# Kernel tuning notes

Hardware: AMD Instinct MI355X
Metric: run time of the kernel (lower is better)

## Reference

```python
import jax, jax.numpy as jnp
import numpy as np

B, N, C = 16384, 4, 512
H = 8
HD = C // H
WIN = 2
SCALE = HD ** -0.5
HID = 2048


def _rel_pos_index(w):
    # same construction as the torch buffer, done in numpy (constant)
    coords = np.stack(np.meshgrid(np.arange(w), np.arange(w), indexing='ij'))  # [2,w,w]
    flat = coords.reshape(2, -1)                      # [2, w*w]
    rel = flat[:, :, None] - flat[:, None, :]         # [2, N, N]
    rel = rel.transpose(1, 2, 0).astype(np.int64)     # [N, N, 2]
    rel[:, :, 0] += w - 1
    rel[:, :, 1] += w - 1
    rel[:, :, 0] *= 2 * w - 1
    return rel.sum(-1)                                # [N, N]

REL_IDX = _rel_pos_index(WIN)


def setup_inputs() -> dict:
    key = jax.random.key(0)
    ks = jax.random.split(key, 8)
    s = lambda fan: 1.0 / np.sqrt(fan)
    return {
        'x': jax.random.normal(ks[0], (B, N, C), jnp.float32),
        'ln_g': jnp.ones((C,), jnp.float32),
        'ln_b': jnp.zeros((C,), jnp.float32),
        'qkv_w': jax.random.normal(ks[1], (3 * C, C), jnp.float32) * s(C),
        'proj_w': jax.random.normal(ks[2], (C, C), jnp.float32) * s(C),
        'proj_b': jnp.zeros((C,), jnp.float32),
        'rpb_table': jax.random.normal(ks[3], ((2 * WIN - 1) ** 2, H), jnp.float32) * 0.02,
        'fc1_w': jax.random.normal(ks[4], (HID, C), jnp.float32) * s(C),
        'fc1_b': jnp.zeros((HID,), jnp.float32),
        'fc2_w': jax.random.normal(ks[5], (C, HID), jnp.float32) * s(HID),
        'fc2_b': jnp.zeros((C,), jnp.float32),
    }


def _layernorm(x, g, b, eps=1e-5):
    mu = jnp.mean(x, axis=-1, keepdims=True)
    var = jnp.mean(jnp.square(x - mu), axis=-1, keepdims=True)
    return (x - mu) * jax.lax.rsqrt(var + eps) * g + b


def reference(x, ln_g, ln_b, qkv_w, proj_w, proj_b, rpb_table, fc1_w, fc1_b, fc2_w, fc2_b):
    # --- attention branch (pre-norm, shared LayerNorm params) ---
    h = _layernorm(x, ln_g, ln_b)
    qkv = h @ qkv_w.T                                  # [B,N,3C]
    qkv = qkv.reshape(B, N, 3, H, HD).transpose(2, 0, 3, 1, 4)  # [3,B,H,N,HD]
    q, k, v = qkv[0], qkv[1], qkv[2]
    attn = jnp.einsum('bhnd,bhmd->bhnm', q, k) * SCALE  # [B,H,N,N]
    bias = rpb_table[REL_IDX.reshape(-1)].reshape(N, N, H).transpose(2, 0, 1)  # [H,N,N]
    attn = jax.nn.softmax(attn + bias[None], axis=-1)
    o = jnp.einsum('bhnm,bhmd->bhnd', attn, v)          # [B,H,N,HD]
    o = o.transpose(0, 2, 1, 3).reshape(B, N, C)
    o = o @ proj_w.T + proj_b
    x = x + o
    # --- MLP branch (same LayerNorm params reused, as in the torch code) ---
    h = _layernorm(x, ln_g, ln_b)
    h = jax.nn.gelu(h @ fc1_w.T + fc1_b, approximate=False)
    h = h @ fc2_w.T + fc2_b
    return x + h
```

## Files before the change

### kernel.cpp

```cpp
#include <hip/hip_runtime.h>
#include <hip/hip_bf16.h>
#include <math.h>

#define BQ   16384
#define CH   512
#define NH   8
#define HID  2048
#define NTOK (BQ*4)

using bf16 = __hip_bfloat16;
typedef __bf16 bf16x8 __attribute__((ext_vector_type(8)));
typedef float  f32x4  __attribute__((ext_vector_type(4)));

__device__ __forceinline__ void gload16(const void* g, void* l) {
    __builtin_amdgcn_global_load_lds(
        (const __attribute__((address_space(1))) void*)g,
        (__attribute__((address_space(3))) void*)l, 16, 0, 0);
}

__global__ __launch_bounds__(256) void packw(const float* __restrict__ Wsrc,
                                             bf16* __restrict__ out, int N, int K) {
    int q = blockIdx.x * 256 + threadIdx.x;
    int NSk = K >> 5;
    int total = (N >> 7) * NSk * 512;
    if (q >= total) return;
    int l  = q & 63;
    int jj = (q >> 6) & 1;
    int w  = (q >> 7) & 3;
    int s  = (q >> 9) % NSk;
    int cb = q / (NSk * 512);
    int row = cb * 128 + w * 32 + jj * 16 + (l >> 2);
    int k   = s * 32 + ((l & 3) ^ ((l >> 3) & 3)) * 8;
    const float* src = Wsrc + (size_t)row * K + k;
    float4 v0 = *(const float4*)src;
    float4 v1 = *(const float4*)(src + 4);
    __align__(16) bf16 t[8];
    t[0] = __float2bfloat16(v0.x); t[1] = __float2bfloat16(v0.y);
    t[2] = __float2bfloat16(v0.z); t[3] = __float2bfloat16(v0.w);
    t[4] = __float2bfloat16(v1.x); t[5] = __float2bfloat16(v1.y);
    t[6] = __float2bfloat16(v1.z); t[7] = __float2bfloat16(v1.w);
    *(uint4*)&out[(size_t)q * 8] = *(const uint4*)t;
}

__global__ __launch_bounds__(256) void ln_kernel(const float* __restrict__ x,
                                                 const float* __restrict__ g,
                                                 const float* __restrict__ b,
                                                 bf16* __restrict__ out) {
    int row  = blockIdx.x * 4 + (threadIdx.x >> 6);
    int lane = threadIdx.x & 63;
    const float* xr = x + (size_t)row * CH;
    int c0 = lane * 8;
    float4 v0 = *(const float4*)&xr[c0];
    float4 v1 = *(const float4*)&xr[c0 + 4];
    float s  = v0.x + v0.y + v0.z + v0.w + v1.x + v1.y + v1.z + v1.w;
    float sq = v0.x*v0.x + v0.y*v0.y + v0.z*v0.z + v0.w*v0.w
             + v1.x*v1.x + v1.y*v1.y + v1.z*v1.z + v1.w*v1.w;
#pragma unroll
    for (int off = 32; off >= 1; off >>= 1) {
        s  += __shfl_xor(s,  off, 64);
        sq += __shfl_xor(sq, off, 64);
    }
    float mu  = s * (1.0f / CH);
    float var = sq * (1.0f / CH) - mu * mu;
    float rs  = rsqrtf(var + 1e-5f);
    float4 g0 = *(const float4*)&g[c0];
    float4 g1 = *(const float4*)&g[c0 + 4];
    float4 b0 = *(const float4*)&b[c0];
    float4 b1 = *(const float4*)&b[c0 + 4];
    __align__(16) bf16 t[8];
    t[0] = __float2bfloat16((v0.x - mu) * rs * g0.x + b0.x);
    t[1] = __float2bfloat16((v0.y - mu) * rs * g0.y + b0.y);
    t[2] = __float2bfloat16((v0.z - mu) * rs * g0.z + b0.z);
    t[3] = __float2bfloat16((v0.w - mu) * rs * g0.w + b0.w);
    t[4] = __float2bfloat16((v1.x - mu) * rs * g1.x + b1.x);
    t[5] = __float2bfloat16((v1.y - mu) * rs * g1.y + b1.y);
    t[6] = __float2bfloat16((v1.z - mu) * rs * g1.z + b1.z);
    t[7] = __float2bfloat16((v1.w - mu) * rs * g1.w + b1.w);
    *(uint4*)&out[(size_t)row * CH + c0] = *(const uint4*)t;
}

template<int EPI>
__global__ __launch_bounds__(256, 3)
void gemm128(const bf16* __restrict__ A, const bf16* __restrict__ Bp,
             int M, int N, int K, int nbx,
             const float* __restrict__ bias,
             const float* resid, float* outF, bf16* __restrict__ outB) {
    __shared__ __align__(16) char lds[32768];
    const int tid  = threadIdx.x;
    const int w    = tid >> 6;
    const int lane = tid & 63;

    const int nb  = gridDim.x;
    const int id  = blockIdx.x;
    const int swz = (id & 7) * (nb >> 3) + (id >> 3);
    const int bx  = swz % nbx, by = swz / nbx;
    const int bm = by * 128, bn = bx * 128;
    const int wrh = w >> 1;
    const int wch = w & 1;
    const int NSk = K >> 5;

    const int rl  = lane >> 2;
    const int kpe = ((lane & 3) ^ ((lane >> 3) & 3)) * 8;
    const bf16* gA0 = A + (size_t)(bm + w * 32 + rl) * K + kpe;
    const bf16* gA1 = gA0 + (size_t)16 * K;
    const bf16* gB = Bp + (size_t)(bn >> 7) * NSk * 4096 + w * 1024 + lane * 8;

    const int kslot = ((lane >> 4) ^ ((lane >> 1) & 3));
    const int aoff = (wrh * 64 + (lane & 15)) * 64 + kslot * 16;
    const int boff = 8192 + (wch * 64 + (lane & 15)) * 64 + kslot * 16;

    f32x4 acc[4][4] = {};

    auto stage = [&](int s) {
        char* base = (char*)lds + (s & 1) * 16384;
        gload16(gA0 + (size_t)s * 32,         base + w * 2048);
        gload16(gA1 + (size_t)s * 32,         base + w * 2048 + 1024);
        gload16(gB  + (size_t)s * 4096,       base + 8192 + w * 2048);
        gload16(gB  + (size_t)s * 4096 + 512, base + 8192 + w * 2048 + 1024);
    };

    auto compute = [&](int slot) {
        const char* base = (const char*)lds + slot * 16384;
        bf16x8 av[4], bv[4];
#pragma unroll
        for (int n = 0; n < 4; ++n)
            bv[n] = *(const bf16x8*)(base + boff + n * 1024);
#pragma unroll
        for (int m = 0; m < 4; ++m)
            av[m] = *(const bf16x8*)(base + aoff + m * 1024);
#pragma unroll
        for (int m = 0; m < 4; ++m)
#pragma unroll
            for (int n = 0; n < 4; ++n)
                acc[m][n] = __builtin_amdgcn_mfma_f32_16x16x32_bf16(av[m], bv[n], acc[m][n], 0, 0, 0);
    };

    stage(0);
    __syncthreads();
    for (int s = 0; s < NSk - 1; ++s) {
        stage(s + 1);
        compute(s & 1);
        __syncthreads();
    }
    compute((NSk - 1) & 1);

    const int erow0 = bm + wrh * 64 + (lane >> 4) * 4;
    const int ecol0 = bn + wch * 64 + (lane & 15);
#pragma unroll
    for (int m = 0; m < 4; ++m) {
#pragma unroll
        for (int n = 0; n < 4; ++n) {
            int col = ecol0 + n * 16;
#pragma unroll
            for (int r = 0; r < 4; ++r) {
                int row = erow0 + m * 16 + r;
                size_t idx = (size_t)row * N + col;
                float v = acc[m][n][r];
                if (EPI == 0) {
                    outB[idx] = __float2bfloat16(v);
                } else if (EPI == 1) {
                    outF[idx] = v + bias[col] + resid[idx];
                } else {
                    float t = v + bias[col];
                    float u = 0.7978845608f * t * (1.0f + 0.044715f * t * t);
                    float e = __expf(2.0f * u);
                    float th = 1.0f - 2.0f / (e + 1.0f);
                    outB[idx] = __float2bfloat16(0.5f * t * (1.0f + th));
                }
            }
        }
    }
}

__global__ __launch_bounds__(256)
void attn_kernel(const bf16* __restrict__ qkv, const float* __restrict__ rpb,
                 bf16* __restrict__ o) {
    __shared__ __align__(16) bf16 sT[4 * 1536];
    __shared__ float sS[NH][4][4];
    __shared__ float sP[NH][4][4];
    int b   = blockIdx.x;
    int tid = threadIdx.x;
    const bf16* src = qkv + (size_t)b * (4 * 1536);
#pragma unroll
    for (int it = 0; it < 3; ++it) {
        int e = (it * 256 + tid) * 8;
        *(uint4*)&sT[e] = *(const uint4*)&src[e];
    }
    __syncthreads();
    if (tid < 128) {
        int h = tid >> 4, i = (tid >> 2) & 3, j = tid & 3;
        const bf16* q = &sT[i * 1536 + h * 64];
        const bf16* k = &sT[j * 1536 + 512 + h * 64];
        float acc = 0.f;
#pragma unroll
        for (int d = 0; d < 64; ++d)
            acc += __bfloat162float(q[d]) * __bfloat162float(k[d]);
        int rel = (((i >> 1) - (j >> 1)) + 1) * 3 + (((i & 1) - (j & 1)) + 1);
        sS[h][i][j] = acc * 0.125f + rpb[rel * NH + h];
    }
    __syncthreads();
    if (tid < 32) {
        int h = tid >> 2, i = tid & 3;
        float s0 = sS[h][i][0], s1 = sS[h][i][1], s2 = sS[h][i][2], s3 = sS[h][i][3];
        float mx = fmaxf(fmaxf(s0, s1), fmaxf(s2, s3));
        float e0 = expf(s0 - mx), e1 = expf(s1 - mx), e2 = expf(s2 - mx), e3 = expf(s3 - mx);
        float inv = 1.f / (e0 + e1 + e2 + e3);
        sP[h][i][0] = e0 * inv; sP[h][i][1] = e1 * inv;
        sP[h][i][2] = e2 * inv; sP[h][i][3] = e3 * inv;
    }
    __syncthreads();
    {
        int h = tid >> 5, tl = tid & 31;
        int d = tl * 2;
        const bf16* v = &sT[1024 + h * 64 + d];
#pragma unroll
        for (int i = 0; i < 4; ++i) {
            float p0 = sP[h][i][0], p1 = sP[h][i][1], p2 = sP[h][i][2], p3 = sP[h][i][3];
            float o0 = p0 * __bfloat162float(v[0])        + p1 * __bfloat162float(v[1536])
                     + p2 * __bfloat162float(v[2 * 1536]) + p3 * __bfloat162float(v[3 * 1536]);
            float o1 = p0 * __bfloat162float(v[1])            + p1 * __bfloat162float(v[1536 + 1])
                     + p2 * __bfloat162float(v[2 * 1536 + 1]) + p3 * __bfloat162float(v[3 * 1536 + 1]);
            __hip_bfloat162 pr;
            pr.x = __float2bfloat16(o0);
            pr.y = __float2bfloat16(o1);
            *(__hip_bfloat162*)&o[(size_t)(b * 4 + i) * CH + h * 64 + d] = pr;
        }
    }
}

extern "C" void kernel_launch(void* const* d_in, const int* in_sizes, int n_in,
                              void* d_out, int out_size, void* d_ws, size_t ws_size,
                              hipStream_t stream) {
    const float* x      = (const float*)d_in[0];
    const float* ln_g   = (const float*)d_in[1];
    const float* ln_b   = (const float*)d_in[2];
    const float* qkv_w  = (const float*)d_in[3];
    const float* proj_w = (const float*)d_in[4];
    const float* proj_b = (const float*)d_in[5];
    const float* rpb    = (const float*)d_in[6];
    const float* fc1_w  = (const float*)d_in[7];
    const float* fc1_b  = (const float*)d_in[8];
    const float* fc2_w  = (const float*)d_in[9];
    const float* fc2_b  = (const float*)d_in[10];
    float* out = (float*)d_out;

    char* ws = (char*)d_ws;
    bf16* wQKV  = (bf16*)ws;  ws += (size_t)1536 * 512 * 2;
    bf16* wPROJ = (bf16*)ws;  ws += (size_t)512  * 512 * 2;
    bf16* wFC1  = (bf16*)ws;  ws += (size_t)2048 * 512 * 2;
    bf16* wFC2  = (bf16*)ws;  ws += (size_t)512 * 2048 * 2;
    bf16* hA    = (bf16*)ws;  ws += (size_t)NTOK * 512 * 2;
    bf16* big   = (bf16*)ws;
    const size_t needed = 6291456ull + 67108864ull + 268435456ull;
    if (ws_size < needed) return;

    packw<<<384, 256, 0, stream>>>(qkv_w,  wQKV, 1536, 512);
    packw<<<128, 256, 0, stream>>>(proj_w, wPROJ, 512, 512);
    packw<<<512, 256, 0, stream>>>(fc1_w,  wFC1, 2048, 512);
    packw<<<512, 256, 0, stream>>>(fc2_w,  wFC2, 512, 2048);

    ln_kernel<<<NTOK / 4, 256, 0, stream>>>(x, ln_g, ln_b, hA);
    gemm128<0><<<dim3(12 * 512), 256, 0, stream>>>(
        hA, wQKV, NTOK, 1536, 512, 12, nullptr, nullptr, nullptr, big);
    attn_kernel<<<BQ, 256, 0, stream>>>(big, rpb, hA);
    gemm128<1><<<dim3(4 * 512), 256, 0, stream>>>(
        hA, wPROJ, NTOK, 512, 512, 4, proj_b, x, out, nullptr);
    ln_kernel<<<NTOK / 4, 256, 0, stream>>>(out, ln_g, ln_b, hA);
    gemm128<2><<<dim3(16 * 512), 256, 0, stream>>>(
        hA, wFC1, NTOK, 2048, 512, 16, fc1_b, nullptr, nullptr, big);
    gemm128<1><<<dim3(4 * 512), 256, 0, stream>>>(
        big, wFC2, NTOK, 512, 2048, 4, fc2_b, out, out, nullptr);
}
```

Measured before the change: 816.7 us.

## Load weight tiles directly to registers and use K=64 stages in GEMM

```diff
diff --git a/kernel.cpp b/kernel.cpp
--- a/kernel.cpp
+++ b/kernel.cpp
@@ -12,25 +12,26 @@
 typedef __bf16 bf16x8 __attribute__((ext_vector_type(8)));
 typedef float  f32x4  __attribute__((ext_vector_type(4)));
 
+#define FENCE() asm volatile("" ::: "memory")
+
 __device__ __forceinline__ void gload16(const void* g, void* l) {
     __builtin_amdgcn_global_load_lds(
         (const __attribute__((address_space(1))) void*)g,
         (__attribute__((address_space(3))) void*)l, 16, 0, 0);
 }
 
-__global__ __launch_bounds__(256) void packw(const float* __restrict__ Wsrc,
+__global__ __launch_bounds__(256) void packb(const float* __restrict__ Wsrc,
                                              bf16* __restrict__ out, int N, int K) {
     int q = blockIdx.x * 256 + threadIdx.x;
-    int NSk = K >> 5;
-    int total = (N >> 7) * NSk * 512;
+    int NSk32 = K >> 5;
+    int total = (N >> 7) * NSk32 * 512;
     if (q >= total) return;
-    int l  = q & 63;
-    int jj = (q >> 6) & 1;
-    int w  = (q >> 7) & 3;
-    int s  = (q >> 9) % NSk;
-    int cb = q / (NSk * 512);
-    int row = cb * 128 + w * 32 + jj * 16 + (l >> 2);
-    int k   = s * 32 + ((l & 3) ^ ((l >> 3) & 3)) * 8;
+    int l   = q & 63;
+    int nt  = (q >> 6) & 7;
+    int s32 = (q >> 9) % NSk32;
+    int cb  = q / (NSk32 * 512);
+    int row = cb * 128 + nt * 16 + (l & 15);
+    int k   = s32 * 32 + (l >> 4) * 8;
     const float* src = Wsrc + (size_t)row * K + k;
     float4 v0 = *(const float4*)src;
     float4 v1 = *(const float4*)(src + 4);
@@ -80,8 +81,8 @@
 }
 
 template<int EPI>
-__global__ __launch_bounds__(256, 3)
-void gemm128(const bf16* __restrict__ A, const bf16* __restrict__ Bp,
+__global__ __launch_bounds__(256, 4)
+void gemmk64(const bf16* __restrict__ A, const bf16* __restrict__ Bp,
              int M, int N, int K, int nbx,
              const float* __restrict__ bias,
              const float* resid, float* outF, bf16* __restrict__ outB) {
@@ -97,52 +98,73 @@
     const int bm = by * 128, bn = bx * 128;
     const int wrh = w >> 1;
     const int wch = w & 1;
-    const int NSk = K >> 5;
+    const int NS    = K >> 6;
+    const int NSk32 = K >> 5;
 
     const int rl  = lane >> 2;
     const int kpe = ((lane & 3) ^ ((lane >> 3) & 3)) * 8;
     const bf16* gA0 = A + (size_t)(bm + w * 32 + rl) * K + kpe;
     const bf16* gA1 = gA0 + (size_t)16 * K;
-    const bf16* gB = Bp + (size_t)(bn >> 7) * NSk * 4096 + w * 1024 + lane * 8;
+    const bf16* gB = Bp + (size_t)(bn >> 7) * NSk32 * 4096 + (wch * 4) * 512 + lane * 8;
 
     const int kslot = ((lane >> 4) ^ ((lane >> 1) & 3));
     const int aoff = (wrh * 64 + (lane & 15)) * 64 + kslot * 16;
-    const int boff = 8192 + (wch * 64 + (lane & 15)) * 64 + kslot * 16;
 
     f32x4 acc[4][4] = {};
-
-    auto stage = [&](int s) {
+    bf16x8 bvA[8], bvB[8];
+
+    auto stageA = [&](int s) {
         char* base = (char*)lds + (s & 1) * 16384;
-        gload16(gA0 + (size_t)s * 32,         base + w * 2048);
-        gload16(gA1 + (size_t)s * 32,         base + w * 2048 + 1024);
-        gload16(gB  + (size_t)s * 4096,       base + 8192 + w * 2048);
-        gload16(gB  + (size_t)s * 4096 + 512, base + 8192 + w * 2048 + 1024);
+        gload16(gA0 + (size_t)s * 64,      base + w * 2048);
+        gload16(gA1 + (size_t)s * 64,      base + w * 2048 + 1024);
+        gload16(gA0 + (size_t)s * 64 + 32, base + 8192 + w * 2048);
+        gload16(gA1 + (size_t)s * 64 + 32, base + 8192 + w * 2048 + 1024);
     };
 
-    auto compute = [&](int slot) {
-        const char* base = (const char*)lds + slot * 16384;
-        bf16x8 av[4], bv[4];
-#pragma unroll
-        for (int n = 0; n < 4; ++n)
-            bv[n] = *(const bf16x8*)(base + boff + n * 1024);
-#pragma unroll
-        for (int m = 0; m < 4; ++m)
-            av[m] = *(const bf16x8*)(base + aoff + m * 1024);
-#pragma unroll
-        for (int m = 0; m < 4; ++m)
-#pragma unroll
-            for (int n = 0; n < 4; ++n)
-                acc[m][n] = __builtin_amdgcn_mfma_f32_16x16x32_bf16(av[m], bv[n], acc[m][n], 0, 0, 0);
-    };
-
-    stage(0);
-    __syncthreads();
-    for (int s = 0; s < NSk - 1; ++s) {
-        stage(s + 1);
-        compute(s & 1);
-        __syncthreads();
-    }
-    compute((NSk - 1) & 1);
+#define LOADB(BV, S) {                                                       \
+    const bf16* _p = gB + (size_t)(2 * (S)) * 4096;                          \
+    BV[0] = *(const bf16x8*)(_p);        BV[1] = *(const bf16x8*)(_p + 512); \
+    BV[2] = *(const bf16x8*)(_p + 1024); BV[3] = *(const bf16x8*)(_p + 1536);\
+    BV[4] = *(const bf16x8*)(_p + 4096);        BV[5] = *(const bf16x8*)(_p + 4096 + 512); \
+    BV[6] = *(const bf16x8*)(_p + 4096 + 1024); BV[7] = *(const bf16x8*)(_p + 4096 + 1536); }
+
+#define COMPUTE(SLOT, BV) {                                                  \
+    const char* _b = (const char*)lds + (size_t)(SLOT) * 16384;              \
+    bf16x8 _av0[4], _av1[4];                                                 \
+    _Pragma("unroll") for (int _m = 0; _m < 4; ++_m) {                       \
+        _av0[_m] = *(const bf16x8*)(_b + aoff + _m * 1024);                  \
+        _av1[_m] = *(const bf16x8*)(_b + 8192 + aoff + _m * 1024); }         \
+    _Pragma("unroll") for (int _m = 0; _m < 4; ++_m)                         \
+    _Pragma("unroll") for (int _n = 0; _n < 4; ++_n)                         \
+        acc[_m][_n] = __builtin_amdgcn_mfma_f32_16x16x32_bf16(_av0[_m], BV[_n], acc[_m][_n], 0, 0, 0); \
+    _Pragma("unroll") for (int _m = 0; _m < 4; ++_m)                         \
+    _Pragma("unroll") for (int _n = 0; _n < 4; ++_n)                         \
+        acc[_m][_n] = __builtin_amdgcn_mfma_f32_16x16x32_bf16(_av1[_m], BV[4 + _n], acc[_m][_n], 0, 0, 0); }
+
+#define WAITV(n) asm volatile("s_waitcnt vmcnt(" #n ")" ::: "memory")
+#define SBAR()   __builtin_amdgcn_s_barrier()
+
+    stageA(0); LOADB(bvA, 0);
+    for (int s = 0; s < NS - 2; s += 2) {
+        stageA(s + 1); LOADB(bvB, s + 1);
+        WAITV(12); SBAR(); FENCE();
+        COMPUTE(s & 1, bvA);
+        FENCE(); SBAR();
+        stageA(s + 2); LOADB(bvA, s + 2);
+        WAITV(12); SBAR(); FENCE();
+        COMPUTE((s + 1) & 1, bvB);
+        FENCE(); SBAR();
+    }
+    stageA(NS - 1); LOADB(bvB, NS - 1);
+    WAITV(12); SBAR(); FENCE();
+    COMPUTE((NS - 2) & 1, bvA);
+    FENCE(); SBAR();
+    WAITV(0); SBAR(); FENCE();
+    COMPUTE((NS - 1) & 1, bvB);
+#undef LOADB
+#undef COMPUTE
+#undef WAITV
+#undef SBAR
 
     const int erow0 = bm + wrh * 64 + (lane >> 4) * 4;
     const int ecol0 = bn + wch * 64 + (lane & 15);
@@ -254,20 +276,20 @@
     const size_t needed = 6291456ull + 67108864ull + 268435456ull;
     if (ws_size < needed) return;
 
-    packw<<<384, 256, 0, stream>>>(qkv_w,  wQKV, 1536, 512);
-    packw<<<128, 256, 0, stream>>>(proj_w, wPROJ, 512, 512);
-    packw<<<512, 256, 0, stream>>>(fc1_w,  wFC1, 2048, 512);
-    packw<<<512, 256, 0, stream>>>(fc2_w,  wFC2, 512, 2048);
+    packb<<<384, 256, 0, stream>>>(qkv_w,  wQKV, 1536, 512);
+    packb<<<128, 256, 0, stream>>>(proj_w, wPROJ, 512, 512);
+    packb<<<512, 256, 0, stream>>>(fc1_w,  wFC1, 2048, 512);
+    packb<<<512, 256, 0, stream>>>(fc2_w,  wFC2, 512, 2048);
 
     ln_kernel<<<NTOK / 4, 256, 0, stream>>>(x, ln_g, ln_b, hA);
-    gemm128<0><<<dim3(12 * 512), 256, 0, stream>>>(
+    gemmk64<0><<<dim3(12 * 512), 256, 0, stream>>>(
         hA, wQKV, NTOK, 1536, 512, 12, nullptr, nullptr, nullptr, big);
     attn_kernel<<<BQ, 256, 0, stream>>>(big, rpb, hA);
-    gemm128<1><<<dim3(4 * 512), 256, 0, stream>>>(
+    gemmk64<1><<<dim3(4 * 512), 256, 0, stream>>>(
         hA, wPROJ, NTOK, 512, 512, 4, proj_b, x, out, nullptr);
     ln_kernel<<<NTOK / 4, 256, 0, stream>>>(out, ln_g, ln_b, hA);
-    gemm128<2><<<dim3(16 * 512), 256, 0, stream>>>(
+    gemmk64<2><<<dim3(16 * 512), 256, 0, stream>>>(
         hA, wFC1, NTOK, 2048, 512, 16, fc1_b, nullptr, nullptr, big);
-    gemm128<1><<<dim3(4 * 512), 256, 0, stream>>>(
+    gemmk64<1><<<dim3(4 * 512), 256, 0, stream>>>(
         big, wFC2, NTOK, 512, 2048, 4, fc2_b, out, out, nullptr);
 }
```

Measured after the change: 2.324 ms. 185% more time.

## Pre-pack activations into MFMA fragment layout and load GEMM operands directly to registers

Applied to the files above, without the earlier changes.

```diff
diff --git a/kernel.cpp b/kernel.cpp
--- a/kernel.cpp
+++ b/kernel.cpp
@@ -12,25 +12,23 @@
 typedef __bf16 bf16x8 __attribute__((ext_vector_type(8)));
 typedef float  f32x4  __attribute__((ext_vector_type(4)));
 
-__device__ __forceinline__ void gload16(const void* g, void* l) {
-    __builtin_amdgcn_global_load_lds(
-        (const __attribute__((address_space(1))) void*)g,
-        (__attribute__((address_space(3))) void*)l, 16, 0, 0);
-}
-
-__global__ __launch_bounds__(256) void packw(const float* __restrict__ Wsrc,
+__device__ __forceinline__ size_t paddr(int row, int col, int NSk) {
+    return ((size_t)(row >> 7) * NSk + (col >> 5)) * 4096
+         + (size_t)(((row & 127) >> 4) * 512 + (((col & 31) >> 3) * 16 + (row & 15)) * 8 + (col & 7));
+}
+
+__global__ __launch_bounds__(256) void packb(const float* __restrict__ Wsrc,
                                              bf16* __restrict__ out, int N, int K) {
     int q = blockIdx.x * 256 + threadIdx.x;
     int NSk = K >> 5;
     int total = (N >> 7) * NSk * 512;
     if (q >= total) return;
-    int l  = q & 63;
-    int jj = (q >> 6) & 1;
-    int w  = (q >> 7) & 3;
-    int s  = (q >> 9) % NSk;
-    int cb = q / (NSk * 512);
-    int row = cb * 128 + w * 32 + jj * 16 + (l >> 2);
-    int k   = s * 32 + ((l & 3) ^ ((l >> 3) & 3)) * 8;
+    int l   = q & 63;
+    int nt  = (q >> 6) & 7;
+    int s32 = (q >> 9) % NSk;
+    int cb  = q / (NSk * 512);
+    int row = cb * 128 + nt * 16 + (l & 15);
+    int k   = s32 * 32 + (l >> 4) * 8;
     const float* src = Wsrc + (size_t)row * K + k;
     float4 v0 = *(const float4*)src;
     float4 v1 = *(const float4*)(src + 4);
@@ -76,16 +74,17 @@
     t[5] = __float2bfloat16((v1.y - mu) * rs * g1.y + b1.y);
     t[6] = __float2bfloat16((v1.z - mu) * rs * g1.z + b1.z);
     t[7] = __float2bfloat16((v1.w - mu) * rs * g1.w + b1.w);
-    *(uint4*)&out[(size_t)row * CH + c0] = *(const uint4*)t;
+    size_t pa = ((size_t)(row >> 7) * 16 + (lane >> 2)) * 4096
+              + (size_t)(((row & 127) >> 4) * 512 + ((lane & 3) * 16 + (row & 15)) * 8);
+    *(uint4*)&out[pa] = *(const uint4*)t;
 }
 
 template<int EPI>
 __global__ __launch_bounds__(256, 3)
-void gemm128(const bf16* __restrict__ A, const bf16* __restrict__ Bp,
-             int M, int N, int K, int nbx,
-             const float* __restrict__ bias,
-             const float* resid, float* outF, bf16* __restrict__ outB) {
-    __shared__ __align__(16) char lds[32768];
+void gemmz(const bf16* __restrict__ Ap, const bf16* __restrict__ Bp,
+           int M, int N, int K, int nbx,
+           const float* __restrict__ bias,
+           const float* resid, float* outF, bf16* __restrict__ outB) {
     const int tid  = threadIdx.x;
     const int w    = tid >> 6;
     const int lane = tid & 63;
@@ -99,53 +98,40 @@
     const int wch = w & 1;
     const int NSk = K >> 5;
 
-    const int rl  = lane >> 2;
-    const int kpe = ((lane & 3) ^ ((lane >> 3) & 3)) * 8;
-    const bf16* gA0 = A + (size_t)(bm + w * 32 + rl) * K + kpe;
-    const bf16* gA1 = gA0 + (size_t)16 * K;
-    const bf16* gB = Bp + (size_t)(bn >> 7) * NSk * 4096 + w * 1024 + lane * 8;
-
-    const int kslot = ((lane >> 4) ^ ((lane >> 1) & 3));
-    const int aoff = (wrh * 64 + (lane & 15)) * 64 + kslot * 16;
-    const int boff = 8192 + (wch * 64 + (lane & 15)) * 64 + kslot * 16;
+    const bf16* gA = Ap + (size_t)(bm >> 7) * NSk * 4096 + (wrh * 4) * 512 + lane * 8;
+    const bf16* gB = Bp + (size_t)(bn >> 7) * NSk * 4096 + (wch * 4) * 512 + lane * 8;
 
     f32x4 acc[4][4] = {};
-
-    auto stage = [&](int s) {
-        char* base = (char*)lds + (s & 1) * 16384;
-        gload16(gA0 + (size_t)s * 32,         base + w * 2048);
-        gload16(gA1 + (size_t)s * 32,         base + w * 2048 + 1024);
-        gload16(gB  + (size_t)s * 4096,       base + 8192 + w * 2048);
-        gload16(gB  + (size_t)s * 4096 + 512, base + 8192 + w * 2048 + 1024);
-    };
-
-    auto compute = [&](int slot) {
-        const char* base = (const char*)lds + slot * 16384;
-        bf16x8 av[4], bv[4];
-#pragma unroll
-        for (int n = 0; n < 4; ++n)
-            bv[n] = *(const bf16x8*)(base + boff + n * 1024);
-#pragma unroll
-        for (int m = 0; m < 4; ++m)
-            av[m] = *(const bf16x8*)(base + aoff + m * 1024);
-#pragma unroll
-        for (int m = 0; m < 4; ++m)
-#pragma unroll
-            for (int n = 0; n < 4; ++n)
-                acc[m][n] = __builtin_amdgcn_mfma_f32_16x16x32_bf16(av[m], bv[n], acc[m][n], 0, 0, 0);
-    };
-
-    stage(0);
-    __syncthreads();
-    for (int s = 0; s < NSk - 1; ++s) {
-        stage(s + 1);
-        compute(s & 1);
-        __syncthreads();
-    }
-    compute((NSk - 1) & 1);
+    bf16x8 aA[4], aB[4], bA[4], bB[4];
+
+#define LOADF(V, BASE, S) {                                   \
+    const bf16* _p = (BASE) + (size_t)(S) * 4096;             \
+    V[0] = *(const bf16x8*)(_p);                              \
+    V[1] = *(const bf16x8*)(_p + 512);                        \
+    V[2] = *(const bf16x8*)(_p + 1024);                       \
+    V[3] = *(const bf16x8*)(_p + 1536); }
+
+#define MFMA16(AV, BV) {                                      \
+    _Pragma("unroll") for (int _m = 0; _m < 4; ++_m)          \
+    _Pragma("unroll") for (int _n = 0; _n < 4; ++_n)          \
+        acc[_m][_n] = __builtin_amdgcn_mfma_f32_16x16x32_bf16(AV[_m], BV[_n], acc[_m][_n], 0, 0, 0); }
+
+    LOADF(aA, gA, 0); LOADF(bA, gB, 0);
+    for (int s = 0; s + 2 < NSk; s += 2) {
+        LOADF(aB, gA, s + 1); LOADF(bB, gB, s + 1);
+        MFMA16(aA, bA);
+        LOADF(aA, gA, s + 2); LOADF(bA, gB, s + 2);
+        MFMA16(aB, bB);
+    }
+    LOADF(aB, gA, NSk - 1); LOADF(bB, gB, NSk - 1);
+    MFMA16(aA, bA);
+    MFMA16(aB, bB);
+#undef LOADF
+#undef MFMA16
 
     const int erow0 = bm + wrh * 64 + (lane >> 4) * 4;
     const int ecol0 = bn + wch * 64 + (lane & 15);
+    const int NSo = N >> 5;
 #pragma unroll
     for (int m = 0; m < 4; ++m) {
 #pragma unroll
@@ -154,18 +140,18 @@
 #pragma unroll
             for (int r = 0; r < 4; ++r) {
                 int row = erow0 + m * 16 + r;
-                size_t idx = (size_t)row * N + col;
                 float v = acc[m][n][r];
                 if (EPI == 0) {
-                    outB[idx] = __float2bfloat16(v);
+                    outB[(size_t)row * N + col] = __float2bfloat16(v);
                 } else if (EPI == 1) {
+                    size_t idx = (size_t)row * N + col;
                     outF[idx] = v + bias[col] + resid[idx];
                 } else {
                     float t = v + bias[col];
                     float u = 0.7978845608f * t * (1.0f + 0.044715f * t * t);
                     float e = __expf(2.0f * u);
                     float th = 1.0f - 2.0f / (e + 1.0f);
-                    outB[idx] = __float2bfloat16(0.5f * t * (1.0f + th));
+                    outB[paddr(row, col, NSo)] = __float2bfloat16(0.5f * t * (1.0f + th));
                 }
             }
         }
@@ -223,7 +209,8 @@
             __hip_bfloat162 pr;
             pr.x = __float2bfloat16(o0);
             pr.y = __float2bfloat16(o1);
-            *(__hip_bfloat162*)&o[(size_t)(b * 4 + i) * CH + h * 64 + d] = pr;
+            int row = b * 4 + i, col = h * 64 + d;
+            *(__hip_bfloat162*)&o[paddr(row, col, 16)] = pr;
         }
     }
 }
@@ -254,20 +241,20 @@
     const size_t needed = 6291456ull + 67108864ull + 268435456ull;
     if (ws_size < needed) return;
 
-    packw<<<384, 256, 0, stream>>>(qkv_w,  wQKV, 1536, 512);
-    packw<<<128, 256, 0, stream>>>(proj_w, wPROJ, 512, 512);
-    packw<<<512, 256, 0, stream>>>(fc1_w,  wFC1, 2048, 512);
-    packw<<<512, 256, 0, stream>>>(fc2_w,  wFC2, 512, 2048);
+    packb<<<384, 256, 0, stream>>>(qkv_w,  wQKV, 1536, 512);
+    packb<<<128, 256, 0, stream>>>(proj_w, wPROJ, 512, 512);
+    packb<<<512, 256, 0, stream>>>(fc1_w,  wFC1, 2048, 512);
+    packb<<<512, 256, 0, stream>>>(fc2_w,  wFC2, 512, 2048);
 
     ln_kernel<<<NTOK / 4, 256, 0, stream>>>(x, ln_g, ln_b, hA);
-    gemm128<0><<<dim3(12 * 512), 256, 0, stream>>>(
+    gemmz<0><<<dim3(12 * 512), 256, 0, stream>>>(
         hA, wQKV, NTOK, 1536, 512, 12, nullptr, nullptr, nullptr, big);
     attn_kernel<<<BQ, 256, 0, stream>>>(big, rpb, hA);
-    gemm128<1><<<dim3(4 * 512), 256, 0, stream>>>(
+    gemmz<1><<<dim3(4 * 512), 256, 0, stream>>>(
         hA, wPROJ, NTOK, 512, 512, 4, proj_b, x, out, nullptr);
     ln_kernel<<<NTOK / 4, 256, 0, stream>>>(out, ln_g, ln_b, hA);
-    gemm128<2><<<dim3(16 * 512), 256, 0, stream>>>(
+    gemmz<2><<<dim3(16 * 512), 256, 0, stream>>>(
         hA, wFC1, NTOK, 2048, 512, 16, fc1_b, nullptr, nullptr, big);
-    gemm128<1><<<dim3(4 * 512), 256, 0, stream>>>(
+    gemmz<1><<<dim3(4 * 512), 256, 0, stream>>>(
         big, wFC2, NTOK, 512, 2048, 4, fc2_b, out, out, nullptr);
 }
```

After: 1.039 ms. 1.27x slower.
